# Kernel optimization log

Hardware: AMD Instinct MI355X
Metric: run time of the kernel (lower is better)

The kernel has to match this reference:

```python
import jax, jax.numpy as jnp
import numpy as np

B, T, C, H = 2, 2048, 1024, 16
SCALE = 0.02

def setup_inputs() -> dict:
    key = jax.random.key(0)
    ks = jax.random.split(key, 6)
    x = jax.random.normal(ks[0], (B, T, C), dtype=jnp.float32)
    Wq = jax.random.normal(ks[1], (C, C), dtype=jnp.float32) * SCALE
    Wk = jax.random.normal(ks[2], (C, C), dtype=jnp.float32) * SCALE
    Wv = jax.random.normal(ks[3], (C, C), dtype=jnp.float32) * SCALE
    Wp = jax.random.normal(ks[4], (C, C), dtype=jnp.float32) * SCALE
    z = jnp.zeros((C,), dtype=jnp.float32)
    return {"x": x, "Wq": Wq, "bq": z, "Wk": Wk, "bk": z, "Wv": Wv, "bv": z, "Wp": Wp, "bp": z}

def reference(x, Wq, bq, Wk, bk, Wv, bv, Wp, bp):
    b, t, c = x.shape
    hd = c // H  # head dim
    def split_heads(y):
        return y.reshape(b, t, H, hd).transpose(0, 2, 1, 3)  # [b,h,t,hd]
    q = split_heads(x @ Wq + bq)
    k = split_heads(x @ Wk + bk)
    v = split_heads(x @ Wv + bv)
    # explicit [b,h,t,t] scores with causal mask (tril), scaled by 1/sqrt(hd)
    att = jnp.einsum('bhqd,bhkd->bhqk', q, k) * (1.0 / jnp.sqrt(jnp.asarray(hd, x.dtype)))
    causal = jnp.tril(jnp.ones((t, t), dtype=bool))
    att = jnp.where(causal[None, None], att, jnp.asarray(-jnp.inf, att.dtype))
    att = jax.nn.softmax(att, axis=-1)
    y = jnp.einsum('bhqk,bhkd->bhqd', att, v)  # [b,h,t,hd]
    y = y.transpose(0, 2, 1, 3).reshape(b, t, c)
    return y @ Wp + bp
```

## Files before the change

### kernel.cpp

```cpp
#include <hip/hip_runtime.h>

typedef unsigned short u16;
typedef short s16x8 __attribute__((ext_vector_type(8)));
typedef unsigned short u16x4 __attribute__((ext_vector_type(4)));
typedef float f32x4 __attribute__((ext_vector_type(4)));

#define Bdim 2
#define Tdim 2048
#define Cdim 1024
#define Hn   16
#define HD   64
#define Mdim (Bdim*Tdim)

static __device__ __forceinline__ u16 f2b(float f) {
  union { float f; unsigned u; } x; x.f = f;
  unsigned r = (x.u + 0x7fffu + ((x.u >> 16) & 1u)) >> 16;
  return (u16)r;
}

static __device__ __forceinline__ unsigned cvt_pk(float lo, float hi) {
  unsigned r;
  asm("v_cvt_pk_bf16_f32 %0, %1, %2" : "=v"(r) : "v"(lo), "v"(hi));
  return r;
}

static __device__ __forceinline__ void gload_lds16(const void* g, void* l) {
  __builtin_amdgcn_global_load_lds((const __attribute__((address_space(1))) void*)g,
                                   (__attribute__((address_space(3))) void*)l, 16, 0, 0);
}

__global__ __launch_bounds__(256) void cast_x_kernel(const float* __restrict__ in,
                                                     u16* __restrict__ out) {
  int i = (blockIdx.x * 256 + threadIdx.x) * 4;
  float4 f = *reinterpret_cast<const float4*>(in + i);
  uint2 o;
  o.x = cvt_pk(f.x, f.y);
  o.y = cvt_pk(f.z, f.w);
  *reinterpret_cast<uint2*>(out + i) = o;
}

__global__ __launch_bounds__(256) void transW_kernel(const float* __restrict__ Wq,
                                                     const float* __restrict__ Wk,
                                                     const float* __restrict__ Wv,
                                                     const float* __restrict__ Wp,
                                                     u16* __restrict__ Wt3,
                                                     u16* __restrict__ Wpt) {
  __shared__ u16 tile[64][72];
  const int z = blockIdx.z;
  const float* W = (z == 0) ? Wq : (z == 1) ? Wk : (z == 2) ? Wv : Wp;
  u16* dst = (z < 3) ? (Wt3 + (size_t)z * Cdim * Cdim) : Wpt;
  const int k0 = blockIdx.y * 64, n0 = blockIdx.x * 64;
  const int tx = threadIdx.x & 15, ty = threadIdx.x >> 4;
#pragma unroll
  for (int p = 0; p < 4; ++p) {
    float4 f = *reinterpret_cast<const float4*>(
        &W[(size_t)(k0 + ty + p * 16) * Cdim + n0 + tx * 4]);
    uint2 o;
    o.x = cvt_pk(f.x, f.y);
    o.y = cvt_pk(f.z, f.w);
    *reinterpret_cast<uint2*>(&tile[ty + p * 16][tx * 4]) = o;
  }
  __syncthreads();
#pragma unroll
  for (int p = 0; p < 4; ++p) {
    const int r = ty + p * 16;
    u16x4 w;
#pragma unroll
    for (int jj = 0; jj < 4; ++jj) w[jj] = tile[tx * 4 + jj][r];
    *reinterpret_cast<u16x4*>(&dst[(size_t)(n0 + r) * Cdim + k0 + tx * 4]) = w;
  }
}

template <int MODE>
__global__ __launch_bounds__(256) void gemm_bf16(
    const u16* __restrict__ A, const u16* __restrict__ Bt,
    const float* __restrict__ b0, const float* __restrict__ b1,
    const float* __restrict__ b2,
    u16* __restrict__ q_out, u16* __restrict__ k_out, u16* __restrict__ v_out,
    float* __restrict__ c_out) {
  __shared__ __attribute__((aligned(16))) u16 As[128 * 32];
  __shared__ __attribute__((aligned(16))) u16 Bs[128 * 32];
  const int tid = threadIdx.x;
  const int lane = tid & 63, wave = tid >> 6;
  const int m0 = blockIdx.y * 128, n0 = blockIdx.x * 128;
  const int wm = (wave >> 1) * 64, wn = (wave & 1) * 64;
  const int lr = lane & 15, lk = (lane >> 4) * 8;
  const int srow = lane >> 2, scol = (lane & 3) * 8;
  f32x4 acc[4][4] = {};
  for (int k0 = 0; k0 < Cdim; k0 += 32) {
    __syncthreads();
#pragma unroll
    for (int i = 0; i < 2; ++i) {
      const int slot = wave * 2 + i;
      const int row = slot * 16 + srow;
      gload_lds16(&A[(size_t)(m0 + row) * Cdim + k0 + scol], (char*)As + slot * 1024);
      gload_lds16(&Bt[(size_t)(n0 + row) * Cdim + k0 + scol], (char*)Bs + slot * 1024);
    }
    __syncthreads();
    s16x8 af[4], bf[4];
#pragma unroll
    for (int i = 0; i < 4; ++i) {
      af[i] = *reinterpret_cast<const s16x8*>(&As[(wm + i * 16 + lr) * 32 + lk]);
      bf[i] = *reinterpret_cast<const s16x8*>(&Bs[(wn + i * 16 + lr) * 32 + lk]);
    }
#pragma unroll
    for (int mi = 0; mi < 4; ++mi)
#pragma unroll
      for (int ni = 0; ni < 4; ++ni)
        acc[mi][ni] = __builtin_amdgcn_mfma_f32_16x16x32_bf16(af[mi], bf[ni], acc[mi][ni], 0, 0, 0);
  }
  const int lc = lane & 15, lr4 = (lane >> 4) * 4;
  if (MODE == 0) {
    const int seg = n0 >> 10;
    const float* bias = (seg == 0) ? b0 : (seg == 1) ? b1 : b2;
    const int nb = n0 & 1023;
    if (seg < 2) {
      u16* dst = (seg == 0) ? q_out : k_out;
#pragma unroll
      for (int mi = 0; mi < 4; ++mi)
#pragma unroll
        for (int ni = 0; ni < 4; ++ni) {
          int mb = m0 + wm + mi * 16 + lr4;
          int n = nb + wn + ni * 16 + lc;
          float bn = bias[n];
          unsigned p01 = cvt_pk(acc[mi][ni][0] + bn, acc[mi][ni][1] + bn);
          unsigned p23 = cvt_pk(acc[mi][ni][2] + bn, acc[mi][ni][3] + bn);
          int b = mb >> 11, t = mb & 2047, h = n >> 6, d = n & 63;
          size_t base = (((size_t)(b * Hn + h)) * Tdim + t) * HD + d;
          dst[base]       = (u16)p01;
          dst[base + 64]  = (u16)(p01 >> 16);
          dst[base + 128] = (u16)p23;
          dst[base + 192] = (u16)(p23 >> 16);
        }
    } else {
#pragma unroll
      for (int mi = 0; mi < 4; ++mi)
#pragma unroll
        for (int ni = 0; ni < 4; ++ni) {
          int mbase = m0 + wm + mi * 16 + lr4;
          int n = nb + wn + ni * 16 + lc;
          float bn = bias[n];
          uint2 w;
          w.x = cvt_pk(acc[mi][ni][0] + bn, acc[mi][ni][1] + bn);
          w.y = cvt_pk(acc[mi][ni][2] + bn, acc[mi][ni][3] + bn);
          int b = mbase >> 11, t = mbase & 2047, h = n >> 6, d = n & 63;
          *reinterpret_cast<uint2*>(
              &v_out[(((size_t)(b * Hn + h)) * HD + d) * Tdim + t]) = w;
        }
    }
  } else {
#pragma unroll
    for (int mi = 0; mi < 4; ++mi)
#pragma unroll
      for (int ni = 0; ni < 4; ++ni)
#pragma unroll
        for (int j = 0; j < 4; ++j) {
          int m = m0 + wm + mi * 16 + lr4 + j;
          int n = n0 + wn + ni * 16 + lc;
          c_out[(size_t)m * Cdim + n] = acc[mi][ni][j] + b0[n];
        }
  }
}

__global__ __launch_bounds__(256) void attn_kernel(const u16* __restrict__ Qh,
                                                   const u16* __restrict__ Kh,
                                                   const u16* __restrict__ Vt,
                                                   u16* __restrict__ Yb) {
  __shared__ __attribute__((aligned(16))) u16 Ks[2][64 * 64];
  __shared__ __attribute__((aligned(16))) u16 Vs[2][64 * 64];
  __shared__ __attribute__((aligned(16))) u16 Ps[4][16 * 64];
  const int id = blockIdx.x;
  const int bh = id & 31;
  const int qblk = 31 - (id >> 5);
  const int tid = threadIdx.x;
  const int wave = tid >> 6, lane = tid & 63;
  const int lr = lane & 15, lg = lane >> 4;
  const int r0 = qblk * 64 + wave * 16;
  const int q_idx = r0 + lr;
  const u16* Qb = Qh + (size_t)bh * Tdim * HD;
  const u16* Kb = Kh + (size_t)bh * Tdim * HD;
  const u16* Vb = Vt + (size_t)bh * HD * Tdim;
  const float SC = 0.18033688011112042f;

  const int c1 = tid + 256;
  const int kr0 = tid >> 3, kc0 = (tid & 7) * 8, kw0 = kr0 * 64 + (kc0 ^ ((kr0 & 7) * 8));
  const int kr1 = c1 >> 3, kc1 = (c1 & 7) * 8, kw1 = kr1 * 64 + (kc1 ^ ((kr1 & 7) * 8));

  s16x8 bQ[2];
#pragma unroll
  for (int ks = 0; ks < 2; ++ks)
    bQ[ks] = *reinterpret_cast<const s16x8*>(&Qb[(size_t)q_idx * HD + ks * 32 + lg * 8]);

  float m = -1e30f, l = 0.f;
  f32x4 o[4];
#pragma unroll
  for (int di = 0; di < 4; ++di) o[di] = (f32x4){0.f, 0.f, 0.f, 0.f};

  s16x8 kg0, kg1, vg0, vg1;
  {
    kg0 = *reinterpret_cast<const s16x8*>(&Kb[(size_t)kr0 * HD + kc0]);
    kg1 = *reinterpret_cast<const s16x8*>(&Kb[(size_t)kr1 * HD + kc1]);
    vg0 = *reinterpret_cast<const s16x8*>(&Vb[(size_t)kr0 * Tdim + kc0]);
    vg1 = *reinterpret_cast<const s16x8*>(&Vb[(size_t)kr1 * Tdim + kc1]);
    *reinterpret_cast<s16x8*>(&Ks[0][kw0]) = kg0;
    *reinterpret_cast<s16x8*>(&Ks[0][kw1]) = kg1;
    *reinterpret_cast<s16x8*>(&Vs[0][kw0]) = vg0;
    *reinterpret_cast<s16x8*>(&Vs[0][kw1]) = vg1;
  }
  __syncthreads();

  const int swl = (lr & 7) * 8;
  for (int kb = 0; kb <= qblk; ++kb) {
    const int cur = kb & 1;
    if (kb < qblk) {
      const int kn = (kb + 1) * 64;
      kg0 = *reinterpret_cast<const s16x8*>(&Kb[(size_t)(kn + kr0) * HD + kc0]);
      kg1 = *reinterpret_cast<const s16x8*>(&Kb[(size_t)(kn + kr1) * HD + kc1]);
      vg0 = *reinterpret_cast<const s16x8*>(&Vb[(size_t)kr0 * Tdim + kn + kc0]);
      vg1 = *reinterpret_cast<const s16x8*>(&Vb[(size_t)kr1 * Tdim + kn + kc1]);
    }
    const int k0 = kb * 64;
    f32x4 st[4] = {};
    __builtin_amdgcn_s_setprio(1);
#pragma unroll
    for (int ni = 0; ni < 4; ++ni)
#pragma unroll
      for (int ks = 0; ks < 2; ++ks) {
        s16x8 aK = *reinterpret_cast<const s16x8*>(
            &Ks[cur][(ni * 16 + lr) * 64 + ((ks * 32 + lg * 8) ^ swl)]);
        st[ni] = __builtin_amdgcn_mfma_f32_16x16x32_bf16(aK, bQ[ks], st[ni], 0, 0, 0);
      }
    __builtin_amdgcn_s_setprio(0);
    if (kb == qblk) {
#pragma unroll
      for (int ni = 0; ni < 4; ++ni)
#pragma unroll
        for (int j = 0; j < 4; ++j)
          if (k0 + ni * 16 + lg * 4 + j > q_idx) st[ni][j] = -1e30f;
    }
    float t4[4];
#pragma unroll
    for (int ni = 0; ni < 4; ++ni)
      t4[ni] = fmaxf(fmaxf(st[ni][0], st[ni][1]), fmaxf(st[ni][2], st[ni][3]));
    float tm = fmaxf(fmaxf(t4[0], t4[1]), fmaxf(t4[2], t4[3]));
    tm = fmaxf(tm, __shfl_xor(tm, 16));
    tm = fmaxf(tm, __shfl_xor(tm, 32));
    const float tms = tm * SC;
    if (!__all(tms <= m + 8.0f)) {
      const float mn = fmaxf(m, tms);
      const float corr = exp2f(m - mn);
      l *= corr;
#pragma unroll
      for (int di = 0; di < 4; ++di)
#pragma unroll
        for (int j = 0; j < 4; ++j) o[di][j] *= corr;
      m = mn;
    }
    float rs = 0.f;
#pragma unroll
    for (int ni = 0; ni < 4; ++ni) {
      float p0 = exp2f(fmaf(st[ni][0], SC, -m));
      float p1 = exp2f(fmaf(st[ni][1], SC, -m));
      float p2 = exp2f(fmaf(st[ni][2], SC, -m));
      float p3 = exp2f(fmaf(st[ni][3], SC, -m));
      st[ni][0] = p0; st[ni][1] = p1; st[ni][2] = p2; st[ni][3] = p3;
      rs += (p0 + p1) + (p2 + p3);
    }
    rs += __shfl_xor(rs, 16);
    rs += __shfl_xor(rs, 32);
    l += rs;
#pragma unroll
    for (int ni = 0; ni < 4; ++ni) {
      uint2 pw;
      pw.x = cvt_pk(st[ni][0], st[ni][1]);
      pw.y = cvt_pk(st[ni][2], st[ni][3]);
      *reinterpret_cast<uint2*>(&Ps[wave][lr * 64 + ((ni * 16 + lg * 4) ^ swl)]) = pw;
    }
    s16x8 bP[2];
#pragma unroll
    for (int ks = 0; ks < 2; ++ks)
      bP[ks] = *reinterpret_cast<const s16x8*>(
          &Ps[wave][lr * 64 + ((ks * 32 + lg * 8) ^ swl)]);
    __builtin_amdgcn_s_setprio(1);
#pragma unroll
    for (int di = 0; di < 4; ++di)
#pragma unroll
      for (int ks = 0; ks < 2; ++ks) {
        s16x8 aV = *reinterpret_cast<const s16x8*>(
            &Vs[cur][(di * 16 + lr) * 64 + ((ks * 32 + lg * 8) ^ swl)]);
        o[di] = __builtin_amdgcn_mfma_f32_16x16x32_bf16(aV, bP[ks], o[di], 0, 0, 0);
      }
    __builtin_amdgcn_s_setprio(0);
    __syncthreads();
    if (kb < qblk) {
      const int nxt = cur ^ 1;
      *reinterpret_cast<s16x8*>(&Ks[nxt][kw0]) = kg0;
      *reinterpret_cast<s16x8*>(&Ks[nxt][kw1]) = kg1;
      *reinterpret_cast<s16x8*>(&Vs[nxt][kw0]) = vg0;
      *reinterpret_cast<s16x8*>(&Vs[nxt][kw1]) = vg1;
    }
    __syncthreads();
  }
  const int b = bh >> 4, h = bh & 15;
  const float rl = 1.0f / l;
#pragma unroll
  for (int di = 0; di < 4; ++di) {
    uint2 w;
    w.x = cvt_pk(o[di][0] * rl, o[di][1] * rl);
    w.y = cvt_pk(o[di][2] * rl, o[di][3] * rl);
    *reinterpret_cast<uint2*>(
        &Yb[((size_t)(b * Tdim + q_idx)) * Cdim + h * 64 + di * 16 + lg * 4]) = w;
  }
}

extern "C" void kernel_launch(void* const* d_in, const int* in_sizes, int n_in,
                              void* d_out, int out_size, void* d_ws, size_t ws_size,
                              hipStream_t stream) {
  const float* x  = (const float*)d_in[0];
  const float* Wq = (const float*)d_in[1];
  const float* bq = (const float*)d_in[2];
  const float* Wk = (const float*)d_in[3];
  const float* bk = (const float*)d_in[4];
  const float* Wv = (const float*)d_in[5];
  const float* bv = (const float*)d_in[6];
  const float* Wp = (const float*)d_in[7];
  const float* bp = (const float*)d_in[8];
  float* out = (float*)d_out;
  char* ws = (char*)d_ws;

  u16* xb  = (u16*)(ws);
  u16* Wt3 = (u16*)(ws + ((size_t)8  << 20));
  u16* Wpt = (u16*)(ws + ((size_t)14 << 20));
  u16* Qh  = (u16*)(ws + ((size_t)16 << 20));
  u16* Kh  = (u16*)(ws + ((size_t)24 << 20));
  u16* Vt  = (u16*)(ws + ((size_t)32 << 20));
  u16* Yb  = (u16*)(ws + ((size_t)48 << 20));

  cast_x_kernel<<<4096, 256, 0, stream>>>(x, xb);
  transW_kernel<<<dim3(16, 16, 4), 256, 0, stream>>>(Wq, Wk, Wv, Wp, Wt3, Wpt);
  gemm_bf16<0><<<dim3(24, 32), 256, 0, stream>>>(xb, Wt3, bq, bk, bv, Qh, Kh, Vt, nullptr);
  attn_kernel<<<1024, 256, 0, stream>>>(Qh, Kh, Vt, Yb);
  gemm_bf16<1><<<dim3(8, 32), 256, 0, stream>>>(Yb, Wpt, bp, nullptr, nullptr,
                                                nullptr, nullptr, nullptr, out);
}
```

Baseline: 209.4 us.

## Read K/V fragments directly from global memory and remap heads across XCDs

The attention kernel no longer stages K and V tiles through double-buffered shared memory with block-wide barriers. Each wave now loads its MFMA operands straight from global memory and relies on the L2 cache for reuse across the four waves. The block-to-head mapping is also permuted so that blocks sharing a head land on the same XCD, improving L2 locality. The change removes LDS traffic and two syncs per iteration, but each wave now issues redundant global loads with exposed latency and no software prefetch.

```diff
diff --git a/kernel.cpp b/kernel.cpp
--- a/kernel.cpp
+++ b/kernel.cpp
@@ -166,11 +166,9 @@
                                                    const u16* __restrict__ Kh,
                                                    const u16* __restrict__ Vt,
                                                    u16* __restrict__ Yb) {
-  __shared__ __attribute__((aligned(16))) u16 Ks[2][64 * 64];
-  __shared__ __attribute__((aligned(16))) u16 Vs[2][64 * 64];
   __shared__ __attribute__((aligned(16))) u16 Ps[4][16 * 64];
   const int id = blockIdx.x;
-  const int bh = id & 31;
+  const int bh = (id & 7) * 4 + ((id >> 3) & 3);
   const int qblk = 31 - (id >> 5);
   const int tid = threadIdx.x;
   const int wave = tid >> 6, lane = tid & 63;
@@ -182,10 +180,6 @@
   const u16* Vb = Vt + (size_t)bh * HD * Tdim;
   const float SC = 0.18033688011112042f;
 
-  const int c1 = tid + 256;
-  const int kr0 = tid >> 3, kc0 = (tid & 7) * 8, kw0 = kr0 * 64 + (kc0 ^ ((kr0 & 7) * 8));
-  const int kr1 = c1 >> 3, kc1 = (c1 & 7) * 8, kw1 = kr1 * 64 + (kc1 ^ ((kr1 & 7) * 8));
-
   s16x8 bQ[2];
 #pragma unroll
   for (int ks = 0; ks < 2; ++ks)
@@ -196,29 +190,8 @@
 #pragma unroll
   for (int di = 0; di < 4; ++di) o[di] = (f32x4){0.f, 0.f, 0.f, 0.f};
 
-  s16x8 kg0, kg1, vg0, vg1;
-  {
-    kg0 = *reinterpret_cast<const s16x8*>(&Kb[(size_t)kr0 * HD + kc0]);
-    kg1 = *reinterpret_cast<const s16x8*>(&Kb[(size_t)kr1 * HD + kc1]);
-    vg0 = *reinterpret_cast<const s16x8*>(&Vb[(size_t)kr0 * Tdim + kc0]);
-    vg1 = *reinterpret_cast<const s16x8*>(&Vb[(size_t)kr1 * Tdim + kc1]);
-    *reinterpret_cast<s16x8*>(&Ks[0][kw0]) = kg0;
-    *reinterpret_cast<s16x8*>(&Ks[0][kw1]) = kg1;
-    *reinterpret_cast<s16x8*>(&Vs[0][kw0]) = vg0;
-    *reinterpret_cast<s16x8*>(&Vs[0][kw1]) = vg1;
-  }
-  __syncthreads();
-
   const int swl = (lr & 7) * 8;
   for (int kb = 0; kb <= qblk; ++kb) {
-    const int cur = kb & 1;
-    if (kb < qblk) {
-      const int kn = (kb + 1) * 64;
-      kg0 = *reinterpret_cast<const s16x8*>(&Kb[(size_t)(kn + kr0) * HD + kc0]);
-      kg1 = *reinterpret_cast<const s16x8*>(&Kb[(size_t)(kn + kr1) * HD + kc1]);
-      vg0 = *reinterpret_cast<const s16x8*>(&Vb[(size_t)kr0 * Tdim + kn + kc0]);
-      vg1 = *reinterpret_cast<const s16x8*>(&Vb[(size_t)kr1 * Tdim + kn + kc1]);
-    }
     const int k0 = kb * 64;
     f32x4 st[4] = {};
     __builtin_amdgcn_s_setprio(1);
@@ -227,7 +200,7 @@
 #pragma unroll
       for (int ks = 0; ks < 2; ++ks) {
         s16x8 aK = *reinterpret_cast<const s16x8*>(
-            &Ks[cur][(ni * 16 + lr) * 64 + ((ks * 32 + lg * 8) ^ swl)]);
+            &Kb[(size_t)(k0 + ni * 16 + lr) * HD + ks * 32 + lg * 8]);
         st[ni] = __builtin_amdgcn_mfma_f32_16x16x32_bf16(aK, bQ[ks], st[ni], 0, 0, 0);
       }
     __builtin_amdgcn_s_setprio(0);
@@ -287,19 +260,10 @@
 #pragma unroll
       for (int ks = 0; ks < 2; ++ks) {
         s16x8 aV = *reinterpret_cast<const s16x8*>(
-            &Vs[cur][(di * 16 + lr) * 64 + ((ks * 32 + lg * 8) ^ swl)]);
+            &Vb[(size_t)(di * 16 + lr) * Tdim + k0 + ks * 32 + lg * 8]);
         o[di] = __builtin_amdgcn_mfma_f32_16x16x32_bf16(aV, bP[ks], o[di], 0, 0, 0);
       }
     __builtin_amdgcn_s_setprio(0);
-    __syncthreads();
-    if (kb < qblk) {
-      const int nxt = cur ^ 1;
-      *reinterpret_cast<s16x8*>(&Ks[nxt][kw0]) = kg0;
-      *reinterpret_cast<s16x8*>(&Ks[nxt][kw1]) = kg1;
-      *reinterpret_cast<s16x8*>(&Vs[nxt][kw0]) = vg0;
-      *reinterpret_cast<s16x8*>(&Vs[nxt][kw1]) = vg1;
-    }
-    __syncthreads();
   }
   const int b = bh >> 4, h = bh & 15;
   const float rl = 1.0f / l;
```

Measured after the change: 311.2 us. +48.6%, slower.
